# Kernel optimization log

Measured on AMD Instinct MI355X. Metric: run time of the kernel, lower is better.

## Reference

```python
import jax, jax.numpy as jnp
import numpy as np

N_SRC, N_TGT, E = 50000, 10000, 150000
D_IN, D_OUT = 512, 512
N_ETYPES, N_NTYPES = 8, 4


def setup_inputs() -> dict:
    key = jax.random.key(0)
    ks = jax.random.split(key, 9)
    scale = 1.0 / np.sqrt(D_IN)
    return {
        "x_src": jax.random.normal(ks[0], (N_SRC, D_IN), jnp.float32),
        "x_target": jax.random.normal(ks[1], (N_TGT, D_IN), jnp.float32),
        "rel_W": jax.random.normal(ks[2], (N_ETYPES, D_IN, D_OUT), jnp.float32) * scale,
        "root_W": jax.random.normal(ks[3], (N_NTYPES, D_IN, D_OUT), jnp.float32) * scale,
        "root_b": jax.random.normal(ks[4], (N_NTYPES, D_OUT), jnp.float32) * scale,
        "edge_src": jax.random.randint(ks[5], (E,), 0, N_SRC, jnp.int64).astype(jnp.int32),
        "edge_dst": jax.random.randint(ks[6], (E,), 0, N_TGT, jnp.int64).astype(jnp.int32),
        "edge_type": jax.random.randint(ks[7], (E,), 0, N_ETYPES, jnp.int64).astype(jnp.int32),
        "target_node_type": jax.random.randint(ks[8], (N_TGT,), 0, N_NTYPES, jnp.int64).astype(jnp.int32),
    }


def reference(x_src, x_target, rel_W, root_W, root_b,
              edge_src, edge_dst, edge_type, target_node_type):
    T = rel_W.shape[0]
    n_tgt = x_target.shape[0]
    # Transform every source node under every relation (grouped GEMM),
    # then gather per edge: msg_e = W_{etype_e} @ x_src[src_e].
    h = jnp.einsum('ni,tio->tno', x_src, rel_W)          # [T, N_src, D_out]
    msg = h[edge_type, edge_src]                          # [E, D_out]
    # PyG aggr='mean' is applied per edge type then SUMMED across types:
    # segment-mean keyed by (dst, etype), empty segments contribute 0.
    seg = edge_dst * T + edge_type                        # [E]
    sums = jax.ops.segment_sum(msg, seg, num_segments=n_tgt * T)
    counts = jax.ops.segment_sum(jnp.ones((msg.shape[0],), msg.dtype), seg,
                                 num_segments=n_tgt * T)
    means = sums / jnp.maximum(counts, 1.0)[:, None]      # [N_tgt*T, D_out]
    out = means.reshape(n_tgt, T, -1).sum(axis=1)         # [N_tgt, D_out]
    # Per-node-type root linear (with bias), selected per target node.
    root = jnp.einsum('ni,tio->nto', x_target, root_W) + root_b[None]  # [N_tgt, NT, D_out]
    root_sel = jnp.take_along_axis(root, target_node_type[:, None, None], axis=1)[:, 0]
    return out + root_sel
```

## Files before the change

### kernel.cpp

```cpp
#include <hip/hip_runtime.h>
#include <hip/hip_bf16.h>

#define D 512
#define T_ETYPES 8
#define NT_TYPES 4
#define K_MAIN 4096
#define K_A 4608
#define K_B 6144
#define SPLITS 6
#define KSPLIT 768
#define BK 64


typedef __attribute__((ext_vector_type(8))) short bf16x8;
typedef __attribute__((ext_vector_type(4))) float f32x4;

__device__ __forceinline__ unsigned short f2bf(float f) {
    union { float f; unsigned u; } u{f};
    unsigned r = u.u + 0x7FFF + ((u.u >> 16) & 1);
    return (unsigned short)(r >> 16);
}
__device__ __forceinline__ float bf2f(unsigned short h) {
    union { unsigned u; float f; } v{(unsigned)h << 16};
    return v.f;
}

__device__ __forceinline__ void gl16(const unsigned short* g, unsigned short* l) {
    __builtin_amdgcn_global_load_lds(
        (const __attribute__((address_space(1))) unsigned int*)g,
        (__attribute__((address_space(3))) unsigned int*)l,
        16, 0, 0);
}

__global__ void convert_weights(const float* __restrict__ relW,
                                const float* __restrict__ rootW,
                                unsigned short* __restrict__ WbT) {
    __shared__ float tile[32][33];
    int c0 = blockIdx.x * 32;
    int o0 = blockIdx.y * 32;
    int tid = threadIdx.x;
#pragma unroll
    for (int it = 0; it < 4; ++it) {
        int idx = it * 256 + tid;
        int oc = idx & 31, cc = idx >> 5;
        int c = c0 + cc, o = o0 + oc;
        float v = (c < K_MAIN) ? relW[(size_t)c * D + o]
                               : rootW[(size_t)(c - K_MAIN) * D + o];
        tile[cc][oc] = v;
    }
    __syncthreads();
#pragma unroll
    for (int it = 0; it < 4; ++it) {
        int idx = it * 256 + tid;
        int cc = idx & 31, oc = idx >> 5;
        int o = o0 + oc, c = c0 + cc;
        int csw = (c & ~63) | (((((c >> 3) & 7) ^ (o & 7))) << 3) | (c & 7);
        WbT[(size_t)o * K_B + csw] = f2bf(tile[cc][oc]);
    }
}

__global__ void hist_kernel(const int* __restrict__ edst, const int* __restrict__ etyp,
                            int* __restrict__ counts, int E) {
    int e = blockIdx.x * 256 + threadIdx.x;
    if (e < E) atomicAdd(&counts[edst[e] * T_ETYPES + etyp[e]], 1);
}

__global__ void scan1(const int* __restrict__ counts, int* __restrict__ partial,
                      int* __restrict__ blockSums, int n) {
    __shared__ int sh[256];
    int tid = threadIdx.x, i = blockIdx.x * 256 + tid;
    int c = (i < n) ? counts[i] : 0;
    int val = c;
    sh[tid] = val; __syncthreads();
#pragma unroll
    for (int off = 1; off < 256; off <<= 1) {
        int add = (tid >= off) ? sh[tid - off] : 0;
        __syncthreads();
        val += add; sh[tid] = val;
        __syncthreads();
    }
    if (i < n) partial[i] = val - c;
    if (tid == 255) blockSums[blockIdx.x] = val;
}

__global__ void scan2(int* __restrict__ blockSums, int nb) {
    __shared__ int sh[512];
    int tid = threadIdx.x;
    int c = (tid < nb) ? blockSums[tid] : 0;
    int val = c;
    sh[tid] = val; __syncthreads();
#pragma unroll
    for (int off = 1; off < 512; off <<= 1) {
        int add = (tid >= off) ? sh[tid - off] : 0;
        __syncthreads();
        val += add; sh[tid] = val;
        __syncthreads();
    }
    if (tid < nb) blockSums[tid] = val - c;
}

__global__ void scan3(const int* __restrict__ partial, const int* __restrict__ blockSums,
                      int* __restrict__ offsets, int* __restrict__ cursors, int n) {
    int i = blockIdx.x * 256 + threadIdx.x;
    if (i < n) {
        int v = partial[i] + blockSums[i >> 8];
        offsets[i] = v;
        cursors[i] = v;
    }
}

__global__ void scatter_kernel(const int* __restrict__ esrc, const int* __restrict__ edst,
                               const int* __restrict__ etyp, int* __restrict__ cursors,
                               int* __restrict__ perm, int E) {
    int e = blockIdx.x * 256 + threadIdx.x;
    if (e < E) {
        int seg = edst[e] * T_ETYPES + etyp[e];
        int pos = atomicAdd(&cursors[seg], 1);
        perm[pos] = esrc[e];
    }
}

__global__ void thist2(const int* __restrict__ tnt, int* __restrict__ bcnt, int M) {
    __shared__ int h[NT_TYPES];
    if (threadIdx.x < NT_TYPES) h[threadIdx.x] = 0;
    __syncthreads();
    int i = blockIdx.x * 256 + threadIdx.x;
    if (i < M) atomicAdd(&h[tnt[i]], 1);
    __syncthreads();
    if (threadIdx.x < NT_TYPES) bcnt[blockIdx.x * NT_TYPES + threadIdx.x] = h[threadIdx.x];
}

__global__ void tprep2(const int* __restrict__ bcnt, int nb,
                       int* __restrict__ boff, int* __restrict__ gstart,
                       int* __restrict__ endv) {
    __shared__ int sb[128 * NT_TYPES];
    __shared__ int gs[NT_TYPES];
    int tid = threadIdx.x;
    for (int i = tid; i < nb * NT_TYPES; i += blockDim.x) sb[i] = bcnt[i];
    __syncthreads();
    if (tid == 0) {
        int s = 0;
        for (int g = 0; g < NT_TYPES; ++g) {
            int tot = 0;
            for (int b = 0; b < nb; ++b) tot += sb[b * NT_TYPES + g];
            gs[g] = s;
            gstart[g] = s;
            endv[g] = s + tot;
            s += ((tot + 127) >> 7) << 7;
        }
        gstart[NT_TYPES] = s;
    }
    __syncthreads();
    if (tid < NT_TYPES) {
        int run = gs[tid];
        for (int b = 0; b < nb; ++b) {
            boff[b * NT_TYPES + tid] = run;
            run += sb[b * NT_TYPES + tid];
        }
    }
}

__global__ void tscatter2(const int* __restrict__ tnt, const int* __restrict__ boff,
                          int* __restrict__ rowperm, int* __restrict__ invperm, int M) {
    __shared__ int h[NT_TYPES];
    if (threadIdx.x < NT_TYPES) h[threadIdx.x] = 0;
    __syncthreads();
    int n = blockIdx.x * 256 + threadIdx.x;
    if (n < M) {
        int g = tnt[n];
        int lr = atomicAdd(&h[g], 1);
        int p = boff[blockIdx.x * NT_TYPES + g] + lr;
        rowperm[p] = n;
        invperm[n] = p;
    }
}

__global__ void segmean(const float* __restrict__ x_src, const int* __restrict__ perm,
                        const int* __restrict__ offsets, const int* __restrict__ counts,
                        const int* __restrict__ invperm,
                        unsigned short* __restrict__ A, int nseg) {
    int seg = blockIdx.x * 4 + (threadIdx.x >> 6);
    if (seg >= nseg) return;
    int lane = threadIdx.x & 63;
    int beg = offsets[seg], cnt = counts[seg];
    float4 a0 = make_float4(0.f, 0.f, 0.f, 0.f);
    float4 a1 = make_float4(0.f, 0.f, 0.f, 0.f);
    for (int i = 0; i < cnt; ++i) {
        int s = perm[beg + i];
        const float4* p = reinterpret_cast<const float4*>(x_src + (size_t)s * D);
        float4 v0 = p[lane * 2], v1 = p[lane * 2 + 1];
        a0.x += v0.x; a0.y += v0.y; a0.z += v0.z; a0.w += v0.w;
        a1.x += v1.x; a1.y += v1.y; a1.z += v1.z; a1.w += v1.w;
    }
    float sc = (cnt > 0) ? 1.0f / (float)cnt : 0.0f;
    uint4 u;
    u.x = (unsigned)f2bf(a0.x * sc) | ((unsigned)f2bf(a0.y * sc) << 16);
    u.y = (unsigned)f2bf(a0.z * sc) | ((unsigned)f2bf(a0.w * sc) << 16);
    u.z = (unsigned)f2bf(a1.x * sc) | ((unsigned)f2bf(a1.y * sc) << 16);
    u.w = (unsigned)f2bf(a1.z * sc) | ((unsigned)f2bf(a1.w * sc) << 16);
    int dst = seg >> 3, t = seg & 7;
    int nrow = invperm[dst];
    int col = t * D + ((lane >> 3) << 6) + (((lane & 7) ^ (nrow & 7)) << 3);
    *reinterpret_cast<uint4*>(A + (size_t)nrow * K_A + col) = u;
}

__global__ void rootfill(const float* __restrict__ x_target, const int* __restrict__ invperm,
                         unsigned short* __restrict__ A, int M) {
    int idx = blockIdx.x * 256 + threadIdx.x;
    if (idx >= M * 64) return;
    int n = idx >> 6;
    int q = idx & 63;
    const float4* p = reinterpret_cast<const float4*>(x_target + (size_t)n * D + q * 8);
    float4 v0 = p[0], v1 = p[1];
    uint4 u;
    u.x = (unsigned)f2bf(v0.x) | ((unsigned)f2bf(v0.y) << 16);
    u.y = (unsigned)f2bf(v0.z) | ((unsigned)f2bf(v0.w) << 16);
    u.z = (unsigned)f2bf(v1.x) | ((unsigned)f2bf(v1.y) << 16);
    u.w = (unsigned)f2bf(v1.z) | ((unsigned)f2bf(v1.w) << 16);
    int prow = invperm[n];
    int col = K_MAIN + ((q >> 3) << 6) + (((q & 7) ^ (prow & 7)) << 3);
    *reinterpret_cast<uint4*>(A + (size_t)prow * K_A + col) = u;
}

__global__ __launch_bounds__(256, 4)
void rgcn_gemm_sk(const unsigned short* __restrict__ A,
                  const unsigned short* __restrict__ WbT,
                  unsigned short* __restrict__ pbuf,
                  const int* __restrict__ gstart, const int* __restrict__ endv,
                  int MBP, int MPc) {
    __shared__ unsigned short As[128 * BK];
    __shared__ unsigned short Bs[128 * BK];
    const int tid = threadIdx.x;

    int d = blockIdx.x;
    int l = d;
    if ((gridDim.x & 7) == 0) {
        int cpx = gridDim.x >> 3;
        l = (d & 7) * cpx + (d >> 3);
    }
    const int nIdx = l & 3;
    const int mz = l >> 2;
    const int mIdx = mz % MBP;
    const int zIdx = mz / MBP;

    const int blockM = mIdx * 128;
    const int blockN = nIdx * 128;
    const int kBase = zIdx * KSPLIT;
    const int g = (blockM >= gstart[1]) + (blockM >= gstart[2]) + (blockM >= gstart[3]);
    const int endRow = endv[g];
    const int rootOff = g * 512;

    const int wid = tid >> 6, lane = tid & 63;
    const int wr = wid >> 1, wc = wid & 1;
    const int lr = lane & 15, lg = lane >> 4;

    f32x4 acc[4][4] = {};

    const unsigned short* Abase = A + (size_t)blockM * K_A + kBase;
    const unsigned short* Bbase = WbT + (size_t)blockN * K_B;

    for (int t = 0; t < KSPLIT / BK; ++t) {
        const int k0 = t * BK;
        const int kc = kBase + k0;
        const int bc = (kc < K_MAIN) ? kc : kc + rootOff;
#pragma unroll
        for (int q = 0; q < 4; ++q) {
            int c = q * 256 + tid;
            gl16(Abase + (size_t)(c >> 3) * K_A + k0 + (c & 7) * 8, &As[c * 8]);
        }
#pragma unroll
        for (int q = 0; q < 4; ++q) {
            int c = q * 256 + tid;
            gl16(Bbase + (size_t)(c >> 3) * K_B + bc + (c & 7) * 8, &Bs[c * 8]);
        }
        __syncthreads();

#pragma unroll
        for (int ks = 0; ks < 2; ++ks) {
            bf16x8 a_frag[4], b_frag[4];
#pragma unroll
            for (int mi = 0; mi < 4; ++mi) {
                int r = wr * 64 + mi * 16 + lr;
                a_frag[mi] = *reinterpret_cast<const bf16x8*>(
                    &As[r * BK + (((ks * 4 + lg) ^ (r & 7)) << 3)]);
            }
#pragma unroll
            for (int ni = 0; ni < 4; ++ni) {
                int cR = wc * 64 + ni * 16 + lr;
                b_frag[ni] = *reinterpret_cast<const bf16x8*>(
                    &Bs[cR * BK + (((ks * 4 + lg) ^ (cR & 7)) << 3)]);
            }
#pragma unroll
            for (int mi = 0; mi < 4; ++mi)
#pragma unroll
                for (int ni = 0; ni < 4; ++ni)
                    acc[mi][ni] = __builtin_amdgcn_mfma_f32_16x16x32_bf16(
                        a_frag[mi], b_frag[ni], acc[mi][ni], 0, 0, 0);
        }
        __syncthreads();
    }

#pragma unroll
    for (int mi = 0; mi < 4; ++mi) {
#pragma unroll
        for (int r = 0; r < 4; ++r) {
            int row = blockM + wr * 64 + mi * 16 + lg * 4 + r;
            if (row < endRow) {
#pragma unroll
                for (int ni = 0; ni < 4; ++ni) {
                    int col = blockN + wc * 64 + ni * 16 + lr;
                    pbuf[((size_t)zIdx * MPc + row) * D + col] = f2bf(acc[mi][ni][r]);
                }
            }
        }
    }
}

__global__ void reduce_bias(const unsigned short* __restrict__ pbuf,
                            const int* __restrict__ rowperm, const int* __restrict__ tnt,
                            const float* __restrict__ root_b,
                            float* __restrict__ out, int MPc) {
    int idx = blockIdx.x * 256 + threadIdx.x;
    if (idx >= MPc * 64) return;
    int nrow = idx >> 6;
    int col = (idx & 63) * 8;
    int orig = rowperm[nrow];
    if (orig < 0) return;
    float s[8] = {0.f, 0.f, 0.f, 0.f, 0.f, 0.f, 0.f, 0.f};
#pragma unroll
    for (int sp = 0; sp < SPLITS; ++sp) {
        uint4 v = *reinterpret_cast<const uint4*>(pbuf + ((size_t)sp * MPc + nrow) * D + col);
        unsigned u[4] = {v.x, v.y, v.z, v.w};
#pragma unroll
        for (int j = 0; j < 4; ++j) {
            s[2 * j]     += bf2f((unsigned short)(u[j] & 0xFFFF));
            s[2 * j + 1] += bf2f((unsigned short)(u[j] >> 16));
        }
    }
    const float* b = root_b + (size_t)tnt[orig] * D + col;
    float4 o0, o1;
    o0.x = s[0] + b[0]; o0.y = s[1] + b[1]; o0.z = s[2] + b[2]; o0.w = s[3] + b[3];
    o1.x = s[4] + b[4]; o1.y = s[5] + b[5]; o1.z = s[6] + b[6]; o1.w = s[7] + b[7];
    float* o = out + (size_t)orig * D + col;
    *reinterpret_cast<float4*>(o) = o0;
    *reinterpret_cast<float4*>(o + 4) = o1;
}

extern "C" void kernel_launch(void* const* d_in, const int* in_sizes, int n_in,
                              void* d_out, int out_size, void* d_ws, size_t ws_size,
                              hipStream_t stream) {
    const float* x_src    = (const float*)d_in[0];
    const float* x_target = (const float*)d_in[1];
    const float* relW     = (const float*)d_in[2];
    const float* rootW    = (const float*)d_in[3];
    const float* rootb    = (const float*)d_in[4];
    const int*   esrc     = (const int*)d_in[5];
    const int*   edst     = (const int*)d_in[6];
    const int*   etyp     = (const int*)d_in[7];
    const int*   tnt      = (const int*)d_in[8];
    float* out = (float*)d_out;

    const int E = in_sizes[5];
    const int M = in_sizes[8];
    const int NSEG = M * T_ETYPES;
    const int NB = (NSEG + 255) / 256;
    const int NBT = (M + 255) / 256;
    const int MBP = (M + 127) / 128 + (NT_TYPES - 1);
    const int MPc = MBP * 128;

    char* ws = (char*)d_ws;
    size_t off = 0;
    unsigned short* Abf = (unsigned short*)(ws + off); off += (size_t)MPc * K_A * 2;
    unsigned short* WbT = (unsigned short*)(ws + off); off += (size_t)D * K_B * 2;
    unsigned short* pb  = (unsigned short*)(ws + off); off += (size_t)SPLITS * MPc * D * 2;
    int* counts    = (int*)(ws + off); off += (size_t)NSEG * 4;
    int* partial   = (int*)(ws + off); off += (size_t)NSEG * 4;
    int* offsets   = (int*)(ws + off); off += (size_t)NSEG * 4;
    int* cursors   = (int*)(ws + off); off += (size_t)NSEG * 4;
    int* blockSums = (int*)(ws + off); off += 512 * 4;
    int* perm      = (int*)(ws + off); off += (size_t)E * 4;
    int* bcnt      = (int*)(ws + off); off += (size_t)NBT * NT_TYPES * 4;
    int* boff      = (int*)(ws + off); off += (size_t)NBT * NT_TYPES * 4;
    int* gstart    = (int*)(ws + off); off += 8 * 4;
    int* endv      = (int*)(ws + off); off += 8 * 4;
    int* rowperm   = (int*)(ws + off); off += (size_t)MPc * 4;
    int* invperm   = (int*)(ws + off); off += (size_t)M * 4;

    hipMemsetAsync(counts, 0, (size_t)NSEG * 4, stream);
    hipMemsetAsync(rowperm, 0xFF, (size_t)MPc * 4, stream);

    convert_weights<<<dim3(K_B / 32, D / 32), 256, 0, stream>>>(relW, rootW, WbT);
    thist2<<<NBT, 256, 0, stream>>>(tnt, bcnt, M);
    tprep2<<<1, 256, 0, stream>>>(bcnt, NBT, boff, gstart, endv);
    tscatter2<<<NBT, 256, 0, stream>>>(tnt, boff, rowperm, invperm, M);
    hist_kernel<<<(E + 255) / 256, 256, 0, stream>>>(edst, etyp, counts, E);
    scan1<<<NB, 256, 0, stream>>>(counts, partial, blockSums, NSEG);
    scan2<<<1, 512, 0, stream>>>(blockSums, NB);
    scan3<<<NB, 256, 0, stream>>>(partial, blockSums, offsets, cursors, NSEG);
    scatter_kernel<<<(E + 255) / 256, 256, 0, stream>>>(esrc, edst, etyp, cursors, perm, E);
    segmean<<<(NSEG + 3) / 4, 256, 0, stream>>>(x_src, perm, offsets, counts, invperm, Abf, NSEG);
    rootfill<<<(M * 64 + 255) / 256, 256, 0, stream>>>(x_target, invperm, Abf, M);
    rgcn_gemm_sk<<<MBP * 4 * SPLITS, 256, 0, stream>>>(Abf, WbT, pb, gstart, endv, MBP, MPc);
    reduce_bias<<<(MPc * 64 + 255) / 256, 256, 0, stream>>>(pb, rowperm, tnt, rootb, out, MPc);
}
```

Baseline: 186.8 us.

## Widen GEMM tile to 128x256 with 512 threads and fuse segmean with rootfill

The split-K GEMM now uses 512-thread blocks, each computing a 128x256 output tile with 8 waves in a 2x4 arrangement. This halves the grid, so each A tile is loaded from global memory half as often. The segment-mean and root-fill kernels are merged into one launch, removing a kernel boundary. The segment-mean loop also processes two edges per iteration with separate accumulators to expose more memory-level parallelism. The trade-offs are a larger LDS footprint per block, possible occupancy limits at launch_bounds(512,4), and fewer blocks to spread across the CUs.

```diff
diff --git a/kernel.cpp b/kernel.cpp
--- a/kernel.cpp
+++ b/kernel.cpp
@@ -175,23 +175,56 @@
     }
 }
 
-__global__ void segmean(const float* __restrict__ x_src, const int* __restrict__ perm,
+__global__ void build_A(const float* __restrict__ x_src, const int* __restrict__ perm,
                         const int* __restrict__ offsets, const int* __restrict__ counts,
-                        const int* __restrict__ invperm,
-                        unsigned short* __restrict__ A, int nseg) {
+                        const int* __restrict__ invperm, const float* __restrict__ x_target,
+                        unsigned short* __restrict__ A, int nseg, int segBlocks, int M) {
+    if ((int)blockIdx.x >= segBlocks) {
+        int idx = ((int)blockIdx.x - segBlocks) * 256 + threadIdx.x;
+        if (idx >= M * 64) return;
+        int n = idx >> 6;
+        int q = idx & 63;
+        const float4* p = reinterpret_cast<const float4*>(x_target + (size_t)n * D + q * 8);
+        float4 v0 = p[0], v1 = p[1];
+        uint4 u;
+        u.x = (unsigned)f2bf(v0.x) | ((unsigned)f2bf(v0.y) << 16);
+        u.y = (unsigned)f2bf(v0.z) | ((unsigned)f2bf(v0.w) << 16);
+        u.z = (unsigned)f2bf(v1.x) | ((unsigned)f2bf(v1.y) << 16);
+        u.w = (unsigned)f2bf(v1.z) | ((unsigned)f2bf(v1.w) << 16);
+        int prow = invperm[n];
+        int col = K_MAIN + ((q >> 3) << 6) + (((q & 7) ^ (prow & 7)) << 3);
+        *reinterpret_cast<uint4*>(A + (size_t)prow * K_A + col) = u;
+        return;
+    }
     int seg = blockIdx.x * 4 + (threadIdx.x >> 6);
     if (seg >= nseg) return;
     int lane = threadIdx.x & 63;
     int beg = offsets[seg], cnt = counts[seg];
     float4 a0 = make_float4(0.f, 0.f, 0.f, 0.f);
     float4 a1 = make_float4(0.f, 0.f, 0.f, 0.f);
-    for (int i = 0; i < cnt; ++i) {
+    float4 b0 = make_float4(0.f, 0.f, 0.f, 0.f);
+    float4 b1 = make_float4(0.f, 0.f, 0.f, 0.f);
+    int i = 0;
+    for (; i + 2 <= cnt; i += 2) {
+        int s0 = perm[beg + i], s1 = perm[beg + i + 1];
+        const float4* p0 = reinterpret_cast<const float4*>(x_src + (size_t)s0 * D);
+        const float4* p1 = reinterpret_cast<const float4*>(x_src + (size_t)s1 * D);
+        float4 x0 = p0[lane * 2], x1 = p0[lane * 2 + 1];
+        float4 y0 = p1[lane * 2], y1 = p1[lane * 2 + 1];
+        a0.x += x0.x; a0.y += x0.y; a0.z += x0.z; a0.w += x0.w;
+        a1.x += x1.x; a1.y += x1.y; a1.z += x1.z; a1.w += x1.w;
+        b0.x += y0.x; b0.y += y0.y; b0.z += y0.z; b0.w += y0.w;
+        b1.x += y1.x; b1.y += y1.y; b1.z += y1.z; b1.w += y1.w;
+    }
+    if (i < cnt) {
         int s = perm[beg + i];
         const float4* p = reinterpret_cast<const float4*>(x_src + (size_t)s * D);
         float4 v0 = p[lane * 2], v1 = p[lane * 2 + 1];
         a0.x += v0.x; a0.y += v0.y; a0.z += v0.z; a0.w += v0.w;
         a1.x += v1.x; a1.y += v1.y; a1.z += v1.z; a1.w += v1.w;
     }
+    a0.x += b0.x; a0.y += b0.y; a0.z += b0.z; a0.w += b0.w;
+    a1.x += b1.x; a1.y += b1.y; a1.z += b1.z; a1.w += b1.w;
     float sc = (cnt > 0) ? 1.0f / (float)cnt : 0.0f;
     uint4 u;
     u.x = (unsigned)f2bf(a0.x * sc) | ((unsigned)f2bf(a0.y * sc) << 16);
@@ -204,32 +237,14 @@
     *reinterpret_cast<uint4*>(A + (size_t)nrow * K_A + col) = u;
 }
 
-__global__ void rootfill(const float* __restrict__ x_target, const int* __restrict__ invperm,
-                         unsigned short* __restrict__ A, int M) {
-    int idx = blockIdx.x * 256 + threadIdx.x;
-    if (idx >= M * 64) return;
-    int n = idx >> 6;
-    int q = idx & 63;
-    const float4* p = reinterpret_cast<const float4*>(x_target + (size_t)n * D + q * 8);
-    float4 v0 = p[0], v1 = p[1];
-    uint4 u;
-    u.x = (unsigned)f2bf(v0.x) | ((unsigned)f2bf(v0.y) << 16);
-    u.y = (unsigned)f2bf(v0.z) | ((unsigned)f2bf(v0.w) << 16);
-    u.z = (unsigned)f2bf(v1.x) | ((unsigned)f2bf(v1.y) << 16);
-    u.w = (unsigned)f2bf(v1.z) | ((unsigned)f2bf(v1.w) << 16);
-    int prow = invperm[n];
-    int col = K_MAIN + ((q >> 3) << 6) + (((q & 7) ^ (prow & 7)) << 3);
-    *reinterpret_cast<uint4*>(A + (size_t)prow * K_A + col) = u;
-}
-
-__global__ __launch_bounds__(256, 4)
+__global__ __launch_bounds__(512, 4)
 void rgcn_gemm_sk(const unsigned short* __restrict__ A,
                   const unsigned short* __restrict__ WbT,
                   unsigned short* __restrict__ pbuf,
                   const int* __restrict__ gstart, const int* __restrict__ endv,
                   int MBP, int MPc) {
     __shared__ unsigned short As[128 * BK];
-    __shared__ unsigned short Bs[128 * BK];
+    __shared__ unsigned short Bs[256 * BK];
     const int tid = threadIdx.x;
 
     int d = blockIdx.x;
@@ -238,20 +253,20 @@
         int cpx = gridDim.x >> 3;
         l = (d & 7) * cpx + (d >> 3);
     }
-    const int nIdx = l & 3;
-    const int mz = l >> 2;
+    const int nIdx = l & 1;
+    const int mz = l >> 1;
     const int mIdx = mz % MBP;
     const int zIdx = mz / MBP;
 
     const int blockM = mIdx * 128;
-    const int blockN = nIdx * 128;
+    const int blockN = nIdx * 256;
     const int kBase = zIdx * KSPLIT;
     const int g = (blockM >= gstart[1]) + (blockM >= gstart[2]) + (blockM >= gstart[3]);
     const int endRow = endv[g];
     const int rootOff = g * 512;
 
     const int wid = tid >> 6, lane = tid & 63;
-    const int wr = wid >> 1, wc = wid & 1;
+    const int wr = wid >> 2, wc = wid & 3;
     const int lr = lane & 15, lg = lane >> 4;
 
     f32x4 acc[4][4] = {};
@@ -264,13 +279,13 @@
         const int kc = kBase + k0;
         const int bc = (kc < K_MAIN) ? kc : kc + rootOff;
 #pragma unroll
+        for (int q = 0; q < 2; ++q) {
+            int c = q * 512 + tid;
+            gl16(Abase + (size_t)(c >> 3) * K_A + k0 + (c & 7) * 8, &As[c * 8]);
+        }
+#pragma unroll
         for (int q = 0; q < 4; ++q) {
-            int c = q * 256 + tid;
-            gl16(Abase + (size_t)(c >> 3) * K_A + k0 + (c & 7) * 8, &As[c * 8]);
-        }
-#pragma unroll
-        for (int q = 0; q < 4; ++q) {
-            int c = q * 256 + tid;
+            int c = q * 512 + tid;
             gl16(Bbase + (size_t)(c >> 3) * K_B + bc + (c & 7) * 8, &Bs[c * 8]);
         }
         __syncthreads();
@@ -367,6 +382,8 @@
     const int NBT = (M + 255) / 256;
     const int MBP = (M + 127) / 128 + (NT_TYPES - 1);
     const int MPc = MBP * 128;
+    const int segBlocks = (NSEG + 3) / 4;
+    const int rootBlocks = (M * 64 + 255) / 256;
 
     char* ws = (char*)d_ws;
     size_t off = 0;
@@ -398,8 +415,8 @@
     scan2<<<1, 512, 0, stream>>>(blockSums, NB);
     scan3<<<NB, 256, 0, stream>>>(partial, blockSums, offsets, cursors, NSEG);
     scatter_kernel<<<(E + 255) / 256, 256, 0, stream>>>(esrc, edst, etyp, cursors, perm, E);
-    segmean<<<(NSEG + 3) / 4, 256, 0, stream>>>(x_src, perm, offsets, counts, invperm, Abf, NSEG);
-    rootfill<<<(M * 64 + 255) / 256, 256, 0, stream>>>(x_target, invperm, Abf, M);
-    rgcn_gemm_sk<<<MBP * 4 * SPLITS, 256, 0, stream>>>(Abf, WbT, pb, gstart, endv, MBP, MPc);
+    build_A<<<segBlocks + rootBlocks, 256, 0, stream>>>(
+        x_src, perm, offsets, counts, invperm, x_target, Abf, NSEG, segBlocks, M);
+    rgcn_gemm_sk<<<MBP * 2 * SPLITS, 512, 0, stream>>>(Abf, WbT, pb, gstart, endv, MBP, MPc);
     reduce_bias<<<(MPc * 64 + 255) / 256, 256, 0, stream>>>(pb, rowperm, tnt, rootb, out, MPc);
 }
```

Measured after the change: 184.6 us. Within noise of the previous version (-1.2%).
